# Kernel tuning notes

Measured on AMD Instinct MI355X. Metric: run time of the kernel, lower is better.

## Reference

```python
import jax, jax.numpy as jnp
import numpy as np

B, C, H, W = 4, 512, 64, 64
CQ = C // 8  # 64 channels for each of query/key projections


def conv1x1(t, w, b):
    # t: [B, Cin, H, W], w: [Cout, Cin], b: [Cout]
    return jnp.einsum('bchw,oc->bohw', t, w) + b[None, :, None, None]


def setup_inputs() -> dict:
    key = jax.random.key(0)
    ks = jax.random.split(key, 12)
    s = 0.05
    return {
        'x':   jax.random.normal(ks[0], (B, C, H, W), jnp.float32),
        'dep': jax.random.normal(ks[1], (B, C, H, W), jnp.float32),
        'wq':  jax.random.normal(ks[2], (CQ, C), jnp.float32) * s,
        'bq':  jnp.zeros((CQ,), jnp.float32),
        'wqd': jax.random.normal(ks[3], (CQ, C), jnp.float32) * s,
        'bqd': jnp.zeros((CQ,), jnp.float32),
        'wk':  jax.random.normal(ks[4], (CQ, C), jnp.float32) * s,
        'bk':  jnp.zeros((CQ,), jnp.float32),
        'wkd': jax.random.normal(ks[5], (CQ, C), jnp.float32) * s,
        'bkd': jnp.zeros((CQ,), jnp.float32),
        'wv':  jax.random.normal(ks[6], (C, C), jnp.float32) * s,
        'bv':  jnp.zeros((C,), jnp.float32),
        'gamma': jnp.full((1,), 0.5, jnp.float32),
    }


def reference(x, dep, wq, bq, wqd, bqd, wk, bk, wkd, bkd, wv, bv, gamma):
    b, c, h, w = x.shape
    n = h * w
    # concatenated RGB+depth query/key projections: [B, 2*CQ, N]
    q = jnp.concatenate([conv1x1(x, wq, bq), conv1x1(dep, wqd, bqd)], axis=1).reshape(b, -1, n)
    k = jnp.concatenate([conv1x1(x, wk, bk), conv1x1(dep, wkd, bkd)], axis=1).reshape(b, -1, n)
    # energy[b, i, j] = sum_d q[b, d, i] * k[b, d, j]  -> [B, N, N]
    energy = jnp.einsum('bdi,bdj->bij', q, k)
    attn = jax.nn.softmax(energy, axis=-1)
    v = conv1x1(x, wv, bv).reshape(b, c, n)  # [B, C, N]
    # out[b, c, i] = sum_j v[b, c, j] * attn[b, i, j]
    out = jnp.einsum('bcj,bij->bci', v, attn).reshape(b, c, h, w)
    return gamma.reshape(()) * out + x
```

## Files before the change

kernel.cpp:

```cpp
#include <hip/hip_runtime.h>


typedef __attribute__((ext_vector_type(8))) short bf16x8;
typedef __attribute__((ext_vector_type(4))) float f32x4;

__device__ __forceinline__ float bf2f(unsigned short u) {
  return __builtin_bit_cast(float, (unsigned int)u << 16);
}
__device__ __forceinline__ unsigned short f2bf(float f) {
  unsigned int u = __builtin_bit_cast(unsigned int, f);
  u = u + 0x7fffu + ((u >> 16) & 1u);
  return (unsigned short)(u >> 16);
}
__device__ __forceinline__ float bflo(unsigned int u) {
  return __builtin_bit_cast(float, u << 16);
}

__device__ __forceinline__ void gld16(const char* g, char* l) {
  __builtin_amdgcn_global_load_lds(
      (const __attribute__((address_space(1))) unsigned int*)g,
      (__attribute__((address_space(3))) unsigned int*)l, 16, 0, 0);
}

__device__ __forceinline__ int detect_fp32_mode(const void* xv) {
  const unsigned int* p = (const unsigned int*)xv;
  const int lane = threadIdx.x & 63;
  const unsigned int w0 = p[lane];
  const unsigned int w1 = p[64 + lane];
  int cnt = 0;
  const unsigned short us[4] = {
      (unsigned short)(w0 & 0xffffu), (unsigned short)(w0 >> 16),
      (unsigned short)(w1 & 0xffffu), (unsigned short)(w1 >> 16)};
#pragma unroll
  for (int h = 0; h < 4; ++h) {
    const float a = fabsf(bf2f(us[h]));
    cnt += (a > 9.0e-13f && a < 32.0f) ? 1 : 0;
  }
#pragma unroll
  for (int mm = 32; mm >= 1; mm >>= 1) cnt += __shfl_xor(cnt, mm, 64);
  return cnt < 220;
}

__global__ __launch_bounds__(256) void prep_kernel(
    const void* wq, const void* bq, const void* wqd, const void* bqd,
    const void* wk, const void* bk, const void* wkd, const void* bkd,
    const void* wv, const void* bv, const void* gam, const void* x,
    unsigned short* __restrict__ Whi, unsigned short* __restrict__ Wlo,
    float* __restrict__ Bcat, float* __restrict__ gamF)
{
  const int fp32mode = detect_fp32_mode(x);
  const int row = blockIdx.x;
  const void* src; const void* bsrc; int srow;
  if (row < 64)       { src = wq;  bsrc = bq;  srow = row; }
  else if (row < 128) { src = wqd; bsrc = bqd; srow = row - 64; }
  else if (row < 192) { src = wk;  bsrc = bk;  srow = row - 128; }
  else if (row < 256) { src = wkd; bsrc = bkd; srow = row - 192; }
  else                { src = wv;  bsrc = bv;  srow = row - 256; }
  for (int c = threadIdx.x; c < 512; c += 256) {
    const float v = fp32mode ? ((const float*)src)[(size_t)srow * 512 + c]
                             : bf2f(((const unsigned short*)src)[(size_t)srow * 512 + c]);
    const unsigned short h = f2bf(v);
    Whi[(size_t)row * 512 + c] = h;
    Wlo[(size_t)row * 512 + c] = f2bf(v - bf2f(h));
  }
  if (threadIdx.x == 0) {
    Bcat[row] = fp32mode ? ((const float*)bsrc)[srow]
                         : bf2f(((const unsigned short*)bsrc)[srow]);
    if (row == 0)
      gamF[0] = fp32mode ? ((const float*)gam)[0]
                         : bf2f(((const unsigned short*)gam)[0]);
  }
}

__device__ __forceinline__ void do_tile2(
    const unsigned short* __restrict__ Whi, const unsigned short* __restrict__ Wlo,
    const float* bsh,
    const unsigned short* Xhi, const unsigned short* Xlo, int fp32mode,
    int wrow0, int kind, int d0,
    int b, int n0, int l15, int quad,
    unsigned short* __restrict__ Qhi, unsigned short* __restrict__ Qlo,
    unsigned short* __restrict__ Kst, unsigned short* __restrict__ Vst)
{
  f32x4 a0, a1;
#pragma unroll
  for (int r = 0; r < 4; ++r) a0[r] = a1[r] = bsh[wrow0 + quad * 4 + r];
  const unsigned short* whi = Whi + (size_t)(wrow0 + l15) * 512;
  const unsigned short* wlo = Wlo + (size_t)(wrow0 + l15) * 512;
  const unsigned short* x0h = Xhi + l15 * 520;
  const unsigned short* x1h = Xhi + (16 + l15) * 520;
  const unsigned short* x0l = Xlo + l15 * 520;
  const unsigned short* x1l = Xlo + (16 + l15) * 520;
#pragma unroll
  for (int ks = 0; ks < 16; ++ks) {
    const int o = ks * 32 + quad * 8;
    const bf16x8 ah = *(const bf16x8*)(whi + o);
    const bf16x8 b0 = *(const bf16x8*)(x0h + o);
    const bf16x8 b1 = *(const bf16x8*)(x1h + o);
    a0 = __builtin_amdgcn_mfma_f32_16x16x32_bf16(ah, b0, a0, 0, 0, 0);
    a1 = __builtin_amdgcn_mfma_f32_16x16x32_bf16(ah, b1, a1, 0, 0, 0);
    if (fp32mode) {
      const bf16x8 al_ = *(const bf16x8*)(wlo + o);
      const bf16x8 c0 = *(const bf16x8*)(x0l + o);
      const bf16x8 c1 = *(const bf16x8*)(x1l + o);
      a0 = __builtin_amdgcn_mfma_f32_16x16x32_bf16(ah, c0, a0, 0, 0, 0);
      a0 = __builtin_amdgcn_mfma_f32_16x16x32_bf16(al_, b0, a0, 0, 0, 0);
      a1 = __builtin_amdgcn_mfma_f32_16x16x32_bf16(ah, c1, a1, 0, 0, 0);
      a1 = __builtin_amdgcn_mfma_f32_16x16x32_bf16(al_, b1, a1, 0, 0, 0);
    }
  }
#pragma unroll
  for (int ns = 0; ns < 2; ++ns) {
    const f32x4 acc = ns ? a1 : a0;
    const int n = n0 + ns * 16 + l15;
    if (kind <= 1) {
      ushort4 h, l;
#pragma unroll
      for (int r = 0; r < 4; ++r) {
        const float f = acc[r];
        const unsigned short hh = f2bf(f);
        ((unsigned short*)&h)[r] = hh;
        ((unsigned short*)&l)[r] = f2bf(f - bf2f(hh));
      }
      if (kind == 0) {
        const size_t base = (((size_t)b << 12) + n) * 128 + d0 + quad * 4;
        *(ushort4*)(Qhi + base) = h;
        *(ushort4*)(Qlo + base) = l;
      } else {
        const int t = n >> 5, j = n & 31, d = d0 + quad * 4;
        char* tb = (char*)Kst + (((size_t)b * 128 + t) << 14);
        const unsigned off =
            ((unsigned)((j * 128 + d) * 2)) ^ ((unsigned)(j & 7) << 4);
        *(ushort4*)(tb + off) = h;
        *(ushort4*)(tb + 8192 + off) = l;
      }
    } else {
      const int t = n >> 5, j = n & 31;
      char* tb = (char*)Vst + (((size_t)b * 128 + t) << 15);
#pragma unroll
      for (int r = 0; r < 4; ++r) {
        const int c = d0 + quad * 4 + r;
        const unsigned off =
            ((unsigned)((c * 32 + j) * 2)) ^ ((unsigned)(c & 7) << 4);
        *(unsigned short*)(tb + off) = f2bf(acc[r]);
      }
    }
  }
}

__global__ __launch_bounds__(512, 4) void proj_kernel(
    const void* __restrict__ x, const void* __restrict__ dep,
    const unsigned short* __restrict__ Whi, const unsigned short* __restrict__ Wlo,
    const float* __restrict__ Bcat,
    unsigned short* __restrict__ Qhi, unsigned short* __restrict__ Qlo,
    unsigned short* __restrict__ Kst, unsigned short* __restrict__ Vst)
{
  __shared__ unsigned short Xhi[32 * 520];
  __shared__ unsigned short Xlo[32 * 520];
  __shared__ float bsh[768];
  const int fp32mode = detect_fp32_mode(x);
  const int tid  = threadIdx.x;
  const int lane = tid & 63;
  const int w    = tid >> 6;
  const int l15  = lane & 15;
  const int quad = lane >> 4;
  const int b  = blockIdx.y;
  const int n0 = blockIdx.x * 32;

  const int cbase = tid >> 4;
  const int nn    = (tid & 15) * 2;

  for (int i = tid; i < 768; i += 512) bsh[i] = Bcat[i];

  for (int r = 0; r < 16; ++r) {
    const int c = cbase + r * 32;
    const size_t off = (((size_t)b * 512 + c) << 12) + n0 + nn;
    float v0, v1;
    if (fp32mode) {
      const float2 f2 = *(const float2*)((const float*)x + off);
      v0 = f2.x; v1 = f2.y;
    } else {
      const unsigned int v2 = *(const unsigned int*)((const unsigned short*)x + off);
      v0 = bflo(v2 & 0xffffu); v1 = bflo(v2 >> 16);
    }
    const unsigned short h0 = f2bf(v0), h1 = f2bf(v1);
    Xhi[nn * 520 + c]       = h0;
    Xhi[(nn + 1) * 520 + c] = h1;
    Xlo[nn * 520 + c]       = f2bf(v0 - bf2f(h0));
    Xlo[(nn + 1) * 520 + c] = f2bf(v1 - bf2f(h1));
  }
  __syncthreads();

  for (int rt = w; rt < 40; rt += 8) {
    if (rt < 4)
      do_tile2(Whi, Wlo, bsh, Xhi, Xlo, fp32mode, rt * 16,             0, rt * 16,
               b, n0, l15, quad, Qhi, Qlo, Kst, Vst);
    else if (rt < 8)
      do_tile2(Whi, Wlo, bsh, Xhi, Xlo, fp32mode, 128 + (rt - 4) * 16, 1, (rt - 4) * 16,
               b, n0, l15, quad, Qhi, Qlo, Kst, Vst);
    else
      do_tile2(Whi, Wlo, bsh, Xhi, Xlo, fp32mode, 256 + (rt - 8) * 16, 2, (rt - 8) * 16,
               b, n0, l15, quad, Qhi, Qlo, Kst, Vst);
  }
  __syncthreads();

  for (int r = 0; r < 16; ++r) {
    const int c = cbase + r * 32;
    const size_t off = (((size_t)b * 512 + c) << 12) + n0 + nn;
    float v0, v1;
    if (fp32mode) {
      const float2 f2 = *(const float2*)((const float*)dep + off);
      v0 = f2.x; v1 = f2.y;
    } else {
      const unsigned int v2 = *(const unsigned int*)((const unsigned short*)dep + off);
      v0 = bflo(v2 & 0xffffu); v1 = bflo(v2 >> 16);
    }
    const unsigned short h0 = f2bf(v0), h1 = f2bf(v1);
    Xhi[nn * 520 + c]       = h0;
    Xhi[(nn + 1) * 520 + c] = h1;
    Xlo[nn * 520 + c]       = f2bf(v0 - bf2f(h0));
    Xlo[(nn + 1) * 520 + c] = f2bf(v1 - bf2f(h1));
  }
  __syncthreads();

  {
    const int rt = w;
    if (rt < 4)
      do_tile2(Whi, Wlo, bsh, Xhi, Xlo, fp32mode, 64 + rt * 16,        0, 64 + rt * 16,
               b, n0, l15, quad, Qhi, Qlo, Kst, Vst);
    else
      do_tile2(Whi, Wlo, bsh, Xhi, Xlo, fp32mode, 192 + (rt - 4) * 16, 1, 64 + (rt - 4) * 16,
               b, n0, l15, quad, Qhi, Qlo, Kst, Vst);
  }
}

__global__ __launch_bounds__(768, 3) void attn_kernel(
    const unsigned short* __restrict__ Qhi, const unsigned short* __restrict__ Qlo,
    const unsigned short* __restrict__ Kst, const unsigned short* __restrict__ Vst,
    const void* __restrict__ x, const float* __restrict__ gamF,
    void* __restrict__ outp)
{
  __shared__ char KL[2][16384];
  __shared__ char VL[2][32768];
  __shared__ unsigned short P[2][64][40];
  __shared__ float lstat[2][4][16];

  const int fp32mode = detect_fp32_mode(x);
  const int tid  = threadIdx.x;
  const int lane = tid & 63;
  const int w    = tid >> 6;
  const int l15  = lane & 15;
  const int quad = lane >> 4;
  const int id   = blockIdx.x;
  const int b    = (id >> 1) & 3;
  const int n0   = (((id >> 3) << 1) | (id & 1)) * 64;

  asm volatile("" :: "v"(fp32mode) : "memory");

  const char* Kb = (const char*)Kst + (((size_t)b * 128) << 14);
  const char* Vb = (const char*)Vst + (((size_t)b * 128) << 15);

  if (w < 4) {
    const int ihE = w >> 1;
    const int jt  = w & 1;
    bf16x8 qh[2][4], ql[2][4];
#pragma unroll
    for (int itq = 0; itq < 2; ++itq) {
      const size_t qb =
          (((size_t)b << 12) + n0 + ihE * 32 + itq * 16 + l15) * 128 + quad * 8;
#pragma unroll
      for (int ds = 0; ds < 4; ++ds) {
        qh[itq][ds] = *(const bf16x8*)(Qhi + qb + ds * 32);
        ql[itq][ds] = *(const bf16x8*)(Qlo + qb + ds * 32);
      }
    }
#pragma unroll
    for (int ch = 0; ch < 4; ++ch) {
      const int c = w + ch * 4;
      gld16(Kb + c * 1024 + lane * 16, &KL[0][c * 1024]);
    }
    float lpart[2] = {0.f, 0.f};

    for (int t = 0; t <= 128; ++t) {
      asm volatile("s_waitcnt vmcnt(0) lgkmcnt(0)" ::: "memory");
      __builtin_amdgcn_sched_barrier(0);
      __builtin_amdgcn_s_barrier();
      __builtin_amdgcn_sched_barrier(0);
      if (t < 128) {
        const int cur = t & 1;
        if (t < 127) {
          const char* src = Kb + ((size_t)(t + 1) << 14);
#pragma unroll
          for (int ch = 0; ch < 4; ++ch) {
            const int c = w + ch * 4;
            gld16(src + c * 1024 + lane * 16, &KL[cur ^ 1][c * 1024]);
          }
        }
        __builtin_amdgcn_sched_barrier(0);
        const int row = jt * 16 + l15;
        const unsigned rsw = (unsigned)(row & 7) << 4;
        const char* kb = &KL[cur][0];
        bf16x8 kh[4], kl[4];
#pragma unroll
        for (int ds = 0; ds < 4; ++ds) {
          const unsigned off = ((unsigned)(row * 256 + quad * 16 + ds * 64)) ^ rsw;
          kh[ds] = *(const bf16x8*)(kb + off);
          kl[ds] = *(const bf16x8*)(kb + 8192 + off);
        }
        f32x4 ea[2], eb[2], ec[2];
#pragma unroll
        for (int itq = 0; itq < 2; ++itq) {
          ea[itq] = (f32x4){0.f, 0.f, 0.f, 0.f};
          eb[itq] = (f32x4){0.f, 0.f, 0.f, 0.f};
          ec[itq] = (f32x4){0.f, 0.f, 0.f, 0.f};
        }
        __builtin_amdgcn_s_setprio(1);
#pragma unroll
        for (int ds = 0; ds < 4; ++ds)
#pragma unroll
          for (int itq = 0; itq < 2; ++itq) {
            ea[itq] = __builtin_amdgcn_mfma_f32_16x16x32_bf16(kh[ds], qh[itq][ds], ea[itq], 0, 0, 0);
            eb[itq] = __builtin_amdgcn_mfma_f32_16x16x32_bf16(kh[ds], ql[itq][ds], eb[itq], 0, 0, 0);
            ec[itq] = __builtin_amdgcn_mfma_f32_16x16x32_bf16(kl[ds], qh[itq][ds], ec[itq], 0, 0, 0);
          }
        __builtin_amdgcn_s_setprio(0);
#pragma unroll
        for (int itq = 0; itq < 2; ++itq) {
          const f32x4 e = (ea[itq] + eb[itq]) + ec[itq];
          const float p0 = __expf(e[0] - 32.0f);
          const float p1 = __expf(e[1] - 32.0f);
          const float p2 = __expf(e[2] - 32.0f);
          const float p3 = __expf(e[3] - 32.0f);
          const unsigned short u0 = f2bf(p0), u1 = f2bf(p1);
          const unsigned short u2 = f2bf(p2), u3 = f2bf(p3);
          lpart[itq] += (bf2f(u0) + bf2f(u1)) + (bf2f(u2) + bf2f(u3));
          unsigned int* dst = (unsigned int*)
              (&P[cur][ihE * 32 + itq * 16 + l15][jt * 16 + quad * 4]);
          dst[0] = (unsigned int)u0 | ((unsigned int)u1 << 16);
          dst[1] = (unsigned int)u2 | ((unsigned int)u3 << 16);
        }
      }
    }
#pragma unroll
    for (int itq = 0; itq < 2; ++itq) {
      float lp = lpart[itq];
      lp += __shfl_xor(lp, 16, 64);
      lp += __shfl_xor(lp, 32, 64);
      if (quad == 0) lstat[jt][ihE * 2 + itq][l15] = lp;
    }
    __syncthreads();
    return;
  }

  const int wv = w - 4;
#pragma unroll
  for (int k = 0; k < 4; ++k) {
    const int c = wv * 4 + k;
    gld16(Vb + c * 1024 + lane * 16, &VL[0][c * 1024]);
  }
  f32x4 acc[4][4];
#pragma unroll
  for (int ct = 0; ct < 4; ++ct)
#pragma unroll
    for (int itv = 0; itv < 4; ++itv) acc[ct][itv] = (f32x4){0.f, 0.f, 0.f, 0.f};

  for (int t = 0; t <= 128; ++t) {
    if (t <= 127)
      asm volatile("s_waitcnt vmcnt(4)" ::: "memory");
    else
      asm volatile("s_waitcnt vmcnt(0)" ::: "memory");
    __builtin_amdgcn_sched_barrier(0);
    __builtin_amdgcn_s_barrier();
    __builtin_amdgcn_sched_barrier(0);
    if (t >= 1) {
      const int pb = (t - 1) & 1;
      bf16x8 pf[4];
#pragma unroll
      for (int itv = 0; itv < 4; ++itv)
        pf[itv] = *(const bf16x8*)(&P[pb][itv * 16 + l15][quad * 8]);
      const char* vb = &VL[pb][0];
      __builtin_amdgcn_s_setprio(1);
#pragma unroll
      for (int ct = 0; ct < 4; ++ct) {
        const int c = wv * 64 + ct * 16 + l15;
        const unsigned off =
            ((unsigned)(c * 64 + quad * 16)) ^ ((unsigned)(c & 7) << 4);
        const bf16x8 va = *(const bf16x8*)(vb + off);
#pragma unroll
        for (int itv = 0; itv < 4; ++itv)
          acc[ct][itv] = __builtin_amdgcn_mfma_f32_16x16x32_bf16(va, pf[itv], acc[ct][itv], 0, 0, 0);
      }
      __builtin_amdgcn_s_setprio(0);
      __builtin_amdgcn_sched_barrier(0);
    }
    if (t < 127) {
      const char* src = Vb + ((size_t)(t + 1) << 15);
#pragma unroll
      for (int k = 0; k < 4; ++k) {
        const int c = wv * 4 + k;
        gld16(src + c * 1024 + lane * 16, &VL[(t + 1) & 1][c * 1024]);
      }
    }
  }
  __syncthreads();

  const float gv = gamF[0];
  float sc[4];
#pragma unroll
  for (int itv = 0; itv < 4; ++itv) {
    const float l = lstat[0][itv][l15] + lstat[1][itv][l15];
    sc[itv] = gv / l;
  }
#pragma unroll
  for (int ct = 0; ct < 4; ++ct)
#pragma unroll
    for (int r = 0; r < 4; ++r) {
      const int c_g = wv * 64 + ct * 16 + quad * 4 + r;
      const size_t brow = ((size_t)b * 512 + c_g) << 12;
#pragma unroll
      for (int itv = 0; itv < 4; ++itv) {
        const size_t addr = brow + n0 + itv * 16 + l15;
        const float o = sc[itv] * acc[ct][itv][r];
        if (fp32mode) {
          ((float*)outp)[addr] = o + ((const float*)x)[addr];
        } else {
          ((unsigned short*)outp)[addr] =
              f2bf(o + bf2f(((const unsigned short*)x)[addr]));
        }
      }
    }
}

extern "C" void kernel_launch(void* const* d_in, const int* in_sizes, int n_in,
                              void* d_out, int out_size, void* d_ws, size_t ws_size,
                              hipStream_t stream) {
  const void* x    = d_in[0];
  const void* dep  = d_in[1];
  const void* wq   = d_in[2];
  const void* bq   = d_in[3];
  const void* wqd  = d_in[4];
  const void* bqd  = d_in[5];
  const void* wk   = d_in[6];
  const void* bk   = d_in[7];
  const void* wkd  = d_in[8];
  const void* bkd  = d_in[9];
  const void* wv   = d_in[10];
  const void* bv   = d_in[11];
  const void* gam  = d_in[12];

  unsigned short* Whi = (unsigned short*)d_ws;
  unsigned short* Wlo = Whi + (size_t)768 * 512;
  float* Bcat = (float*)(Wlo + (size_t)768 * 512);
  float* gamF = Bcat + 768;
  unsigned short* Qhi = (unsigned short*)((char*)d_ws + ((size_t)2 << 20));
  unsigned short* Qlo = (unsigned short*)((char*)d_ws + ((size_t)6 << 20));
  unsigned short* Kst = (unsigned short*)((char*)d_ws + ((size_t)10 << 20));
  unsigned short* Vst = (unsigned short*)((char*)d_ws + ((size_t)18 << 20));

  prep_kernel<<<768, 256, 0, stream>>>(wq, bq, wqd, bqd, wk, bk, wkd, bkd,
                                       wv, bv, gam, x, Whi, Wlo, Bcat, gamF);
  proj_kernel<<<dim3(128, 4), 512, 0, stream>>>(x, dep, Whi, Wlo, Bcat,
                                                Qhi, Qlo, Kst, Vst);
  attn_kernel<<<256, 768, 0, stream>>>(Qhi, Qlo, Kst, Vst, x, gamF, d_out);
}
```

Measured before the change: 362.4 us.

## Stage projection outputs in LDS and write them out coalesced; split MFMA accumulators

The projection kernel now writes Q, K and V tiles into shared-memory staging buffers and then copies them to global memory with coalesced 16-byte stores. Before, it scattered 2- and 8-byte stores directly to global memory. The hi/lo split-precision MFMA chain is split into three independent accumulators that are summed at the end, which shortens the dependency chain between MFMAs. The X tile row stride changes from 520 to 522 to alter the LDS bank mapping. The extra 64KB of shared memory lowers the occupancy hint from 4 to 2 blocks per CU, and the summation order changes the fp32 rounding slightly.

Result: slower. 451.0 us (+24.5%).

```diff
diff --git a/kernel.cpp b/kernel.cpp
--- a/kernel.cpp
+++ b/kernel.cpp
@@ -77,41 +77,45 @@
     const float* bsh,
     const unsigned short* Xhi, const unsigned short* Xlo, int fp32mode,
     int wrow0, int kind, int d0,
-    int b, int n0, int l15, int quad,
-    unsigned short* __restrict__ Qhi, unsigned short* __restrict__ Qlo,
-    unsigned short* __restrict__ Kst, unsigned short* __restrict__ Vst)
+    int l15, int quad,
+    char* __restrict__ QT, char* __restrict__ KT, char* __restrict__ VT)
 {
-  f32x4 a0, a1;
-#pragma unroll
-  for (int r = 0; r < 4; ++r) a0[r] = a1[r] = bsh[wrow0 + quad * 4 + r];
+  f32x4 A0, A1, B0, B1, C0, C1;
+#pragma unroll
+  for (int r = 0; r < 4; ++r) {
+    A0[r] = A1[r] = bsh[wrow0 + quad * 4 + r];
+    B0[r] = B1[r] = C0[r] = C1[r] = 0.f;
+  }
   const unsigned short* whi = Whi + (size_t)(wrow0 + l15) * 512;
   const unsigned short* wlo = Wlo + (size_t)(wrow0 + l15) * 512;
-  const unsigned short* x0h = Xhi + l15 * 520;
-  const unsigned short* x1h = Xhi + (16 + l15) * 520;
-  const unsigned short* x0l = Xlo + l15 * 520;
-  const unsigned short* x1l = Xlo + (16 + l15) * 520;
+  const unsigned short* x0h = Xhi + l15 * 522;
+  const unsigned short* x1h = Xhi + (16 + l15) * 522;
+  const unsigned short* x0l = Xlo + l15 * 522;
+  const unsigned short* x1l = Xlo + (16 + l15) * 522;
 #pragma unroll
   for (int ks = 0; ks < 16; ++ks) {
     const int o = ks * 32 + quad * 8;
     const bf16x8 ah = *(const bf16x8*)(whi + o);
     const bf16x8 b0 = *(const bf16x8*)(x0h + o);
     const bf16x8 b1 = *(const bf16x8*)(x1h + o);
-    a0 = __builtin_amdgcn_mfma_f32_16x16x32_bf16(ah, b0, a0, 0, 0, 0);
-    a1 = __builtin_amdgcn_mfma_f32_16x16x32_bf16(ah, b1, a1, 0, 0, 0);
+    A0 = __builtin_amdgcn_mfma_f32_16x16x32_bf16(ah, b0, A0, 0, 0, 0);
+    A1 = __builtin_amdgcn_mfma_f32_16x16x32_bf16(ah, b1, A1, 0, 0, 0);
     if (fp32mode) {
       const bf16x8 al_ = *(const bf16x8*)(wlo + o);
       const bf16x8 c0 = *(const bf16x8*)(x0l + o);
       const bf16x8 c1 = *(const bf16x8*)(x1l + o);
-      a0 = __builtin_amdgcn_mfma_f32_16x16x32_bf16(ah, c0, a0, 0, 0, 0);
-      a0 = __builtin_amdgcn_mfma_f32_16x16x32_bf16(al_, b0, a0, 0, 0, 0);
-      a1 = __builtin_amdgcn_mfma_f32_16x16x32_bf16(ah, c1, a1, 0, 0, 0);
-      a1 = __builtin_amdgcn_mfma_f32_16x16x32_bf16(al_, b1, a1, 0, 0, 0);
-    }
-  }
+      B0 = __builtin_amdgcn_mfma_f32_16x16x32_bf16(ah, c0, B0, 0, 0, 0);
+      C0 = __builtin_amdgcn_mfma_f32_16x16x32_bf16(al_, b0, C0, 0, 0, 0);
+      B1 = __builtin_amdgcn_mfma_f32_16x16x32_bf16(ah, c1, B1, 0, 0, 0);
+      C1 = __builtin_amdgcn_mfma_f32_16x16x32_bf16(al_, b1, C1, 0, 0, 0);
+    }
+  }
+  const f32x4 a0 = fp32mode ? (A0 + B0) + C0 : A0;
+  const f32x4 a1 = fp32mode ? (A1 + B1) + C1 : A1;
 #pragma unroll
   for (int ns = 0; ns < 2; ++ns) {
     const f32x4 acc = ns ? a1 : a0;
-    const int n = n0 + ns * 16 + l15;
+    const int n = ns * 16 + l15;
     if (kind <= 1) {
       ushort4 h, l;
 #pragma unroll
@@ -121,41 +125,39 @@
         ((unsigned short*)&h)[r] = hh;
         ((unsigned short*)&l)[r] = f2bf(f - bf2f(hh));
       }
+      const unsigned lin = (unsigned)(n * 256 + (d0 + quad * 4) * 2);
       if (kind == 0) {
-        const size_t base = (((size_t)b << 12) + n) * 128 + d0 + quad * 4;
-        *(ushort4*)(Qhi + base) = h;
-        *(ushort4*)(Qlo + base) = l;
+        *(ushort4*)(QT + lin) = h;
+        *(ushort4*)(QT + 8192 + lin) = l;
       } else {
-        const int t = n >> 5, j = n & 31, d = d0 + quad * 4;
-        char* tb = (char*)Kst + (((size_t)b * 128 + t) << 14);
-        const unsigned off =
-            ((unsigned)((j * 128 + d) * 2)) ^ ((unsigned)(j & 7) << 4);
-        *(ushort4*)(tb + off) = h;
-        *(ushort4*)(tb + 8192 + off) = l;
+        const unsigned off = lin ^ ((unsigned)(n & 7) << 4);
+        *(ushort4*)(KT + off) = h;
+        *(ushort4*)(KT + 8192 + off) = l;
       }
     } else {
-      const int t = n >> 5, j = n & 31;
-      char* tb = (char*)Vst + (((size_t)b * 128 + t) << 15);
 #pragma unroll
       for (int r = 0; r < 4; ++r) {
         const int c = d0 + quad * 4 + r;
         const unsigned off =
-            ((unsigned)((c * 32 + j) * 2)) ^ ((unsigned)(c & 7) << 4);
-        *(unsigned short*)(tb + off) = f2bf(acc[r]);
-      }
-    }
-  }
-}
-
-__global__ __launch_bounds__(512, 4) void proj_kernel(
+            ((unsigned)(c * 64 + n * 2)) ^ ((unsigned)(c & 7) << 4);
+        *(unsigned short*)(VT + off) = f2bf(acc[r]);
+      }
+    }
+  }
+}
+
+__global__ __launch_bounds__(512, 2) void proj_kernel(
     const void* __restrict__ x, const void* __restrict__ dep,
     const unsigned short* __restrict__ Whi, const unsigned short* __restrict__ Wlo,
     const float* __restrict__ Bcat,
     unsigned short* __restrict__ Qhi, unsigned short* __restrict__ Qlo,
     unsigned short* __restrict__ Kst, unsigned short* __restrict__ Vst)
 {
-  __shared__ unsigned short Xhi[32 * 520];
-  __shared__ unsigned short Xlo[32 * 520];
+  __shared__ unsigned short Xhi[32 * 522];
+  __shared__ unsigned short Xlo[32 * 522];
+  __shared__ char QT[16384];
+  __shared__ char KT[16384];
+  __shared__ char VT[32768];
   __shared__ float bsh[768];
   const int fp32mode = detect_fp32_mode(x);
   const int tid  = threadIdx.x;
@@ -164,7 +166,8 @@
   const int l15  = lane & 15;
   const int quad = lane >> 4;
   const int b  = blockIdx.y;
-  const int n0 = blockIdx.x * 32;
+  const int t  = blockIdx.x;
+  const int n0 = t * 32;
 
   const int cbase = tid >> 4;
   const int nn    = (tid & 15) * 2;
@@ -183,26 +186,34 @@
       v0 = bflo(v2 & 0xffffu); v1 = bflo(v2 >> 16);
     }
     const unsigned short h0 = f2bf(v0), h1 = f2bf(v1);
-    Xhi[nn * 520 + c]       = h0;
-    Xhi[(nn + 1) * 520 + c] = h1;
-    Xlo[nn * 520 + c]       = f2bf(v0 - bf2f(h0));
-    Xlo[(nn + 1) * 520 + c] = f2bf(v1 - bf2f(h1));
+    Xhi[nn * 522 + c]       = h0;
+    Xhi[(nn + 1) * 522 + c] = h1;
+    Xlo[nn * 522 + c]       = f2bf(v0 - bf2f(h0));
+    Xlo[(nn + 1) * 522 + c] = f2bf(v1 - bf2f(h1));
   }
   __syncthreads();
 
   for (int rt = w; rt < 40; rt += 8) {
     if (rt < 4)
       do_tile2(Whi, Wlo, bsh, Xhi, Xlo, fp32mode, rt * 16,             0, rt * 16,
-               b, n0, l15, quad, Qhi, Qlo, Kst, Vst);
+               l15, quad, QT, KT, VT);
     else if (rt < 8)
       do_tile2(Whi, Wlo, bsh, Xhi, Xlo, fp32mode, 128 + (rt - 4) * 16, 1, (rt - 4) * 16,
-               b, n0, l15, quad, Qhi, Qlo, Kst, Vst);
+               l15, quad, QT, KT, VT);
     else
       do_tile2(Whi, Wlo, bsh, Xhi, Xlo, fp32mode, 256 + (rt - 8) * 16, 2, (rt - 8) * 16,
-               b, n0, l15, quad, Qhi, Qlo, Kst, Vst);
+               l15, quad, QT, KT, VT);
   }
   __syncthreads();
 
+  {
+    char* vdst = (char*)Vst + (((size_t)b * 128 + t) << 15);
+#pragma unroll
+    for (int i = 0; i < 4; ++i) {
+      const int off = i * 8192 + tid * 16;
+      *(uint4*)(vdst + off) = *(const uint4*)(VT + off);
+    }
+  }
   for (int r = 0; r < 16; ++r) {
     const int c = cbase + r * 32;
     const size_t off = (((size_t)b * 512 + c) << 12) + n0 + nn;
@@ -215,10 +226,10 @@
       v0 = bflo(v2 & 0xffffu); v1 = bflo(v2 >> 16);
     }
     const unsigned short h0 = f2bf(v0), h1 = f2bf(v1);
-    Xhi[nn * 520 + c]       = h0;
-    Xhi[(nn + 1) * 520 + c] = h1;
-    Xlo[nn * 520 + c]       = f2bf(v0 - bf2f(h0));
-    Xlo[(nn + 1) * 520 + c] = f2bf(v1 - bf2f(h1));
+    Xhi[nn * 522 + c]       = h0;
+    Xhi[(nn + 1) * 522 + c] = h1;
+    Xlo[nn * 522 + c]       = f2bf(v0 - bf2f(h0));
+    Xlo[(nn + 1) * 522 + c] = f2bf(v1 - bf2f(h1));
   }
   __syncthreads();
 
@@ -226,10 +237,23 @@
     const int rt = w;
     if (rt < 4)
       do_tile2(Whi, Wlo, bsh, Xhi, Xlo, fp32mode, 64 + rt * 16,        0, 64 + rt * 16,
-               b, n0, l15, quad, Qhi, Qlo, Kst, Vst);
+               l15, quad, QT, KT, VT);
     else
       do_tile2(Whi, Wlo, bsh, Xhi, Xlo, fp32mode, 192 + (rt - 4) * 16, 1, 64 + (rt - 4) * 16,
-               b, n0, l15, quad, Qhi, Qlo, Kst, Vst);
+               l15, quad, QT, KT, VT);
+  }
+  __syncthreads();
+
+  {
+    char* kdst = (char*)Kst + (((size_t)b * 128 + t) << 14);
+#pragma unroll
+    for (int i = 0; i < 2; ++i) {
+      const int off = i * 8192 + tid * 16;
+      *(uint4*)(kdst + off) = *(const uint4*)(KT + off);
+    }
+    const size_t qoff = ((((size_t)b << 12) + n0) * 128) * 2;
+    *(uint4*)((char*)Qhi + qoff + tid * 16) = *(const uint4*)(QT + tid * 16);
+    *(uint4*)((char*)Qlo + qoff + tid * 16) = *(const uint4*)(QT + 8192 + tid * 16);
   }
 }
 
```
